# Optimization experiments

Hardware: AMD Instinct MI355X
Metric: run time of the kernel (lower is better)

Reference implementation:

```python
import jax, jax.numpy as jnp
import numpy as np

NUM_HEADS = 16
N_QUBITS = 8  # both attention d_k and FFN qubit count
LN_EPS = 1e-5


def setup_inputs() -> dict:
    key = jax.random.key(0)
    ks = jax.random.split(key, 8)
    B, S, E, F = 8, 4096, 128, 2048
    return {
        "x": jax.random.normal(ks[0], (B, S, E), dtype=jnp.float32),
        "theta_attn": jax.random.normal(ks[1], (N_QUBITS,), dtype=jnp.float32),
        "phi_ffn": jax.random.normal(ks[2], (N_QUBITS,), dtype=jnp.float32),
        "w1": jax.random.normal(ks[3], (F, N_QUBITS), dtype=jnp.float32) * (1.0 / np.sqrt(N_QUBITS)),
        "b1": jax.random.normal(ks[4], (F,), dtype=jnp.float32) * 0.01,
        "w2": jax.random.normal(ks[5], (E, F), dtype=jnp.float32) * (1.0 / np.sqrt(F)),
        "b2": jax.random.normal(ks[6], (E,), dtype=jnp.float32) * 0.01,
        "gamma1": jnp.ones((E,), dtype=jnp.float32),
        "beta1": jnp.zeros((E,), dtype=jnp.float32),
        "gamma2": jnp.ones((E,), dtype=jnp.float32),
        "beta2": jnp.zeros((E,), dtype=jnp.float32),
    }


def _layernorm(y, g, b):
    m = jnp.mean(y, axis=-1, keepdims=True)
    v = jnp.var(y, axis=-1, keepdims=True)
    return (y - m) * jax.lax.rsqrt(v + LN_EPS) * g + b


def _quantum_attn(x, theta):
    # RX(x_k)RX(theta_k) per wire -> per-wire <Z>=cos(x_k+theta_k); CNOT chain + ring
    # maps Z_j -> Z_0..Z_j (j>=1) and Z_0 -> Z_0..Z_{n-1} (Heisenberg picture),
    # so outputs are cumulative products of cosines within each head.
    B, S, E = x.shape
    a = x.reshape(B, S, NUM_HEADS, N_QUBITS) + theta  # (B,S,H,8)
    cp = jnp.cumprod(jnp.cos(a), axis=-1)
    out = jnp.concatenate([cp[..., -1:], cp[..., 1:]], axis=-1)  # wire0 gets full product
    return out.reshape(B, S, E)


def _quantum_ffn(x, phi):
    # RY(phi_j)RX(x_j)|0> -> <Z_j> = cos(phi_j)*cos(x_j); encoder only reads first N_QUBITS feats
    return jnp.cos(phi) * jnp.cos(x[..., :N_QUBITS])  # (B,S,8)


def reference(x, theta_attn, phi_ffn, w1, b1, w2, b2, gamma1, beta1, gamma2, beta2):
    attn = _quantum_attn(x, theta_attn)
    x1 = _layernorm(x + attn, gamma1, beta1)  # dropout is identity in eval
    q = _quantum_ffn(x1, phi_ffn)
    h = jax.nn.relu(jnp.einsum('bsq,fq->bsf', q, w1) + b1)
    ffn = jnp.einsum('bsf,ef->bse', h, w2) + b2
    return _layernorm(x1 + ffn, gamma2, beta2)
```

## Files before the change

### kernel.cpp

```cpp
#include <hip/hip_runtime.h>
#include <hip/hip_bf16.h>

typedef __attribute__((ext_vector_type(8))) short short8;
typedef __attribute__((ext_vector_type(4))) float f32x4;
typedef __attribute__((ext_vector_type(4))) int int4v;

#define LN_EPS 1e-5f

__device__ __forceinline__ unsigned short bf16rn(float f) {
    unsigned int u = __builtin_bit_cast(unsigned int, f);
    u = u + 0x7fffu + ((u >> 16) & 1u);
    return (unsigned short)(u >> 16);
}

__device__ __forceinline__ unsigned cvt_pk(float lo, float hi) {
    unsigned r;
    asm("v_cvt_pk_bf16_f32 %0, %1, %2" : "=v"(r) : "v"(lo), "v"(hi));
    return r;
}

__global__ __launch_bounds__(256) void k_prep(const float* __restrict__ w2,
                                              const float* __restrict__ w1,
                                              const float* __restrict__ b1,
                                              unsigned short* __restrict__ w2b,
                                              unsigned short* __restrict__ w1p) {
    const int bid = blockIdx.x;
    if (bid < 256) {
        int i = (bid * 256 + threadIdx.x) * 4;
        float4 v = *(const float4*)(w2 + i);
        ushort4 r;
        r.x = bf16rn(v.x); r.y = bf16rn(v.y); r.z = bf16rn(v.z); r.w = bf16rn(v.w);
        *(ushort4*)(w2b + i) = r;
    } else {
        int f = (bid - 256) * 256 + threadIdx.x;
        float4 wa = *(const float4*)(w1 + (size_t)f * 8);
        float4 wb = *(const float4*)(w1 + (size_t)f * 8 + 4);
        short8 r0, r1;
        r0[0] = (short)bf16rn(wa.x); r0[1] = (short)bf16rn(wa.y);
        r0[2] = (short)bf16rn(wa.z); r0[3] = (short)bf16rn(wa.w);
        r0[4] = (short)bf16rn(wb.x); r0[5] = (short)bf16rn(wb.y);
        r0[6] = (short)bf16rn(wb.z); r0[7] = (short)bf16rn(wb.w);
        r1 = short8{0, 0, 0, 0, 0, 0, 0, 0};
        r1[0] = (short)bf16rn(b1[f]);
        short8 z = short8{0, 0, 0, 0, 0, 0, 0, 0};
        unsigned short* row = w1p + (size_t)f * 32;
        *(short8*)(row) = r0;
        *(short8*)(row + 8) = r1;
        *(short8*)(row + 16) = z;
        *(short8*)(row + 24) = z;
    }
}

__global__ __launch_bounds__(256) void k_pre(const float* __restrict__ x,
                                             const float* __restrict__ theta,
                                             const float* __restrict__ phi,
                                             const float* __restrict__ gamma1,
                                             const float* __restrict__ beta1,
                                             float* __restrict__ x1,
                                             unsigned short* __restrict__ qpad) {
    const int tid = threadIdx.x;
    const int g = tid >> 4, li = tid & 15;
    const int tok = blockIdx.x * 16 + g;

    const float* xr = x + (size_t)tok * 128 + li * 8;
    float4 va = *(const float4*)xr;
    float4 vb = *(const float4*)(xr + 4);
    float v[8] = {va.x, va.y, va.z, va.w, vb.x, vb.y, vb.z, vb.w};

    float c[8];
#pragma unroll
    for (int k = 0; k < 8; ++k) c[k] = __cosf(v[k] + theta[k]);
    float cp[8];
    cp[0] = c[0];
#pragma unroll
    for (int k = 1; k < 8; ++k) cp[k] = cp[k - 1] * c[k];

    float y[8];
    y[0] = v[0] + cp[7];
#pragma unroll
    for (int k = 1; k < 8; ++k) y[k] = v[k] + cp[k];

    float s1 = 0.f, s2 = 0.f;
#pragma unroll
    for (int k = 0; k < 8; ++k) { s1 += y[k]; s2 += y[k] * y[k]; }
#pragma unroll
    for (int m = 1; m < 16; m <<= 1) {
        s1 += __shfl_xor(s1, m);
        s2 += __shfl_xor(s2, m);
    }
    float mean = s1 * (1.f / 128.f);
    float var = s2 * (1.f / 128.f) - mean * mean;
    float rs = rsqrtf(var + LN_EPS);

    float4 ga = *(const float4*)(gamma1 + li * 8);
    float4 gb = *(const float4*)(gamma1 + li * 8 + 4);
    float4 ba = *(const float4*)(beta1 + li * 8);
    float4 bb = *(const float4*)(beta1 + li * 8 + 4);
    float gam[8] = {ga.x, ga.y, ga.z, ga.w, gb.x, gb.y, gb.z, gb.w};
    float bet[8] = {ba.x, ba.y, ba.z, ba.w, bb.x, bb.y, bb.z, bb.w};

    float o[8];
#pragma unroll
    for (int k = 0; k < 8; ++k) o[k] = (y[k] - mean) * rs * gam[k] + bet[k];

    float* x1r = x1 + (size_t)tok * 128 + li * 8;
    *(float4*)x1r = make_float4(o[0], o[1], o[2], o[3]);
    *(float4*)(x1r + 4) = make_float4(o[4], o[5], o[6], o[7]);

    if (li == 0) {
        short8 qr;
#pragma unroll
        for (int k = 0; k < 8; ++k)
            qr[k] = (short)bf16rn(__cosf(phi[k]) * __cosf(o[k]));
        *(short8*)(qpad + (size_t)tok * 32) = qr;
    } else if (li < 4) {
        short8 z = short8{0, 0, 0, 0, 0, 0, 0, 0};
        if (li == 1) z[0] = (short)0x3F80;
        *(short8*)(qpad + (size_t)tok * 32 + li * 8) = z;
    }
}

__global__ __launch_bounds__(512, 4) void k_ffn(const float* __restrict__ x1,
                                                const unsigned short* __restrict__ qpad,
                                                const unsigned short* __restrict__ w2b,
                                                const unsigned short* __restrict__ w1p,
                                                const float* __restrict__ b2,
                                                const float* __restrict__ g2,
                                                const float* __restrict__ be2,
                                                float* __restrict__ out) {
    const int tid = threadIdx.x;
    const int wv = tid >> 6;
    const int kh = wv >> 2;
    const int sub = wv & 3;
    const int nh = sub & 1;
    const int mw = sub >> 1;
    const int lane = tid & 63;
    const int li = lane & 15;
    const int lg = lane >> 4;
    const int Tb = blockIdx.x * 64;
    const int lt0 = mw * 32;
    const int t0 = Tb + lt0;

    __shared__ __align__(16) char smem[65536 + 1024];
    unsigned short* Bs = (unsigned short*)smem;
    float (*red)[132] = (float(*)[132])smem;
    float (*sums)[4] = (float(*)[4])(smem + 65536);

    short8 qf[2];
#pragma unroll
    for (int mt = 0; mt < 2; ++mt)
        qf[mt] = *(const short8*)(qpad + (size_t)(t0 + mt * 16 + li) * 32 + lg * 8);

    const int arow0 = (8 * (li >> 2) + (li & 3)) * 32 + lg * 8;

    f32x4 acc[2][4];
#pragma unroll
    for (int mt = 0; mt < 2; ++mt)
#pragma unroll
        for (int nt = 0; nt < 4; ++nt) acc[mt][nt] = f32x4{0.f, 0.f, 0.f, 0.f};

    const int srow = lane >> 3;
    const int scs = (lane & 7) ^ srow;

    auto stage = [&](int buf, int kb_local) {
        const int kb = kh * 1024 + kb_local;
#pragma unroll
        for (int r = 0; r < 4; ++r) {
            const int e0 = r * 32 + sub * 8;
            const unsigned short* src =
                w2b + (size_t)(e0 + srow) * 2048 + kb + scs * 8;
            unsigned short* dst = Bs + (kh * 2 + buf) * 8192 + e0 * 64;
            __builtin_amdgcn_global_load_lds(
                (const __attribute__((address_space(1))) unsigned int*)src,
                (__attribute__((address_space(3))) unsigned int*)dst,
                16, 0, 0);
        }
    };

    stage(0, 0);
    __syncthreads();

    const f32x4 zero4 = f32x4{0.f, 0.f, 0.f, 0.f};

    for (int kbi = 0; kbi < 16; ++kbi) {
        const int buf = kbi & 1;
        if (kbi < 15) stage(buf ^ 1, (kbi + 1) * 64);

#pragma unroll
        for (int kk = 0; kk < 2; ++kk) {
            const int f = kh * 1024 + kbi * 64 + kk * 32;

            const unsigned short* wbase = w1p + (size_t)f * 32;
            short8 A0 = *(const short8*)(wbase + arow0);
            short8 A1 = *(const short8*)(wbase + arow0 + 128);

            const int cs = (kk * 4 + lg) ^ (li & 7);
            const unsigned short* basep =
                Bs + (kh * 2 + buf) * 8192 + (nh * 64 + li) * 64 + cs * 8;
            short8 bfr[4];
#pragma unroll
            for (int nt = 0; nt < 4; ++nt)
                bfr[nt] = *(const short8*)(basep + nt * 1024);

#pragma unroll
            for (int mt = 0; mt < 2; ++mt) {
                f32x4 p0 = __builtin_amdgcn_mfma_f32_16x16x32_bf16(A0, qf[mt], zero4, 0, 0, 0);
                f32x4 p1 = __builtin_amdgcn_mfma_f32_16x16x32_bf16(A1, qf[mt], zero4, 0, 0, 0);
#pragma unroll
                for (int r = 0; r < 4; ++r) {
                    p0[r] = fmaxf(p0[r], 0.f);
                    p1[r] = fmaxf(p1[r], 0.f);
                }
                int4v ai = {(int)cvt_pk(p0[0], p0[1]), (int)cvt_pk(p0[2], p0[3]),
                            (int)cvt_pk(p1[0], p1[1]), (int)cvt_pk(p1[2], p1[3])};
                short8 a2 = __builtin_bit_cast(short8, ai);
#pragma unroll
                for (int nt = 0; nt < 4; ++nt)
                    acc[mt][nt] = __builtin_amdgcn_mfma_f32_16x16x32_bf16(a2, bfr[nt], acc[mt][nt], 0, 0, 0);
            }
        }
        __syncthreads();
    }

    if (kh == 1) {
#pragma unroll
        for (int mt = 0; mt < 2; ++mt)
#pragma unroll
            for (int nt = 0; nt < 4; ++nt)
#pragma unroll
                for (int r = 0; r < 4; ++r)
                    red[lt0 + mt * 16 + lg * 4 + r][nh * 64 + nt * 16 + li] = acc[mt][nt][r];
    }
    __syncthreads();

    float b2v[4], g2v[4], be2v[4];
    if (kh == 0) {
#pragma unroll
        for (int nt = 0; nt < 4; ++nt) {
            int e = nh * 64 + nt * 16 + li;
            b2v[nt] = b2[e]; g2v[nt] = g2[e]; be2v[nt] = be2[e];
        }
#pragma unroll
        for (int mt = 0; mt < 2; ++mt) {
#pragma unroll
            for (int r = 0; r < 4; ++r) {
                const int ltok = lt0 + mt * 16 + lg * 4 + r;
                const int tok = Tb + ltok;
                const float* x1r = x1 + (size_t)tok * 128 + nh * 64 + li;
                float s1 = 0.f, s2 = 0.f;
#pragma unroll
                for (int nt = 0; nt < 4; ++nt) {
                    float v = acc[mt][nt][r] + red[ltok][nh * 64 + nt * 16 + li] +
                              b2v[nt] + x1r[nt * 16];
                    acc[mt][nt][r] = v;
                    s1 += v; s2 += v * v;
                }
#pragma unroll
                for (int m = 1; m < 16; m <<= 1) {
                    s1 += __shfl_xor(s1, m);
                    s2 += __shfl_xor(s2, m);
                }
                if (li == 0) {
                    sums[ltok][nh * 2 + 0] = s1;
                    sums[ltok][nh * 2 + 1] = s2;
                }
            }
        }
    }
    __syncthreads();

    if (kh == 0) {
#pragma unroll
        for (int mt = 0; mt < 2; ++mt) {
#pragma unroll
            for (int r = 0; r < 4; ++r) {
                const int ltok = lt0 + mt * 16 + lg * 4 + r;
                const int tok = Tb + ltok;
                float s1 = sums[ltok][0] + sums[ltok][2];
                float s2 = sums[ltok][1] + sums[ltok][3];
                float mean = s1 * (1.f / 128.f);
                float var = s2 * (1.f / 128.f) - mean * mean;
                float rs = rsqrtf(var + LN_EPS);
                float* orow = out + (size_t)tok * 128 + nh * 64 + li;
#pragma unroll
                for (int nt = 0; nt < 4; ++nt)
                    orow[nt * 16] = (acc[mt][nt][r] - mean) * rs * g2v[nt] + be2v[nt];
            }
        }
    }
}

extern "C" void kernel_launch(void* const* d_in, const int* in_sizes, int n_in,
                              void* d_out, int out_size, void* d_ws, size_t ws_size,
                              hipStream_t stream) {
    const float* x      = (const float*)d_in[0];
    const float* theta  = (const float*)d_in[1];
    const float* phi    = (const float*)d_in[2];
    const float* w1     = (const float*)d_in[3];
    const float* b1     = (const float*)d_in[4];
    const float* w2     = (const float*)d_in[5];
    const float* b2     = (const float*)d_in[6];
    const float* gamma1 = (const float*)d_in[7];
    const float* beta1  = (const float*)d_in[8];
    const float* gamma2 = (const float*)d_in[9];
    const float* beta2  = (const float*)d_in[10];
    float* out = (float*)d_out;

    char* ws = (char*)d_ws;
    unsigned short* w2b  = (unsigned short*)ws;
    unsigned short* w1p  = (unsigned short*)(ws + (512 << 10));
    unsigned short* qpad = (unsigned short*)(ws + (1 << 20));

    k_prep<<<264, 256, 0, stream>>>(w2, w1, b1, w2b, w1p);
    k_pre<<<2048, 256, 0, stream>>>(x, theta, phi, gamma1, beta1, out, qpad);
    k_ffn<<<512, 512, 0, stream>>>(out, qpad, w2b, w1p, b2, gamma2, beta2, out);
}
```

Measured before the change: 58.16 us.

## Merge weight prep into pre kernel and software-pipeline FFN A-fragment loads

```diff
diff --git a/kernel.cpp b/kernel.cpp
--- a/kernel.cpp
+++ b/kernel.cpp
@@ -17,38 +17,6 @@
     unsigned r;
     asm("v_cvt_pk_bf16_f32 %0, %1, %2" : "=v"(r) : "v"(lo), "v"(hi));
     return r;
-}
-
-__global__ __launch_bounds__(256) void k_prep(const float* __restrict__ w2,
-                                              const float* __restrict__ w1,
-                                              const float* __restrict__ b1,
-                                              unsigned short* __restrict__ w2b,
-                                              unsigned short* __restrict__ w1p) {
-    const int bid = blockIdx.x;
-    if (bid < 256) {
-        int i = (bid * 256 + threadIdx.x) * 4;
-        float4 v = *(const float4*)(w2 + i);
-        ushort4 r;
-        r.x = bf16rn(v.x); r.y = bf16rn(v.y); r.z = bf16rn(v.z); r.w = bf16rn(v.w);
-        *(ushort4*)(w2b + i) = r;
-    } else {
-        int f = (bid - 256) * 256 + threadIdx.x;
-        float4 wa = *(const float4*)(w1 + (size_t)f * 8);
-        float4 wb = *(const float4*)(w1 + (size_t)f * 8 + 4);
-        short8 r0, r1;
-        r0[0] = (short)bf16rn(wa.x); r0[1] = (short)bf16rn(wa.y);
-        r0[2] = (short)bf16rn(wa.z); r0[3] = (short)bf16rn(wa.w);
-        r0[4] = (short)bf16rn(wb.x); r0[5] = (short)bf16rn(wb.y);
-        r0[6] = (short)bf16rn(wb.z); r0[7] = (short)bf16rn(wb.w);
-        r1 = short8{0, 0, 0, 0, 0, 0, 0, 0};
-        r1[0] = (short)bf16rn(b1[f]);
-        short8 z = short8{0, 0, 0, 0, 0, 0, 0, 0};
-        unsigned short* row = w1p + (size_t)f * 32;
-        *(short8*)(row) = r0;
-        *(short8*)(row + 8) = r1;
-        *(short8*)(row + 16) = z;
-        *(short8*)(row + 24) = z;
-    }
 }
 
 __global__ __launch_bounds__(256) void k_pre(const float* __restrict__ x,
@@ -56,11 +24,47 @@
                                              const float* __restrict__ phi,
                                              const float* __restrict__ gamma1,
                                              const float* __restrict__ beta1,
+                                             const float* __restrict__ w1,
+                                             const float* __restrict__ b1,
+                                             const float* __restrict__ w2,
                                              float* __restrict__ x1,
-                                             unsigned short* __restrict__ qpad) {
+                                             unsigned short* __restrict__ qpad,
+                                             unsigned short* __restrict__ w2b,
+                                             unsigned short* __restrict__ w1p) {
     const int tid = threadIdx.x;
+    const int bid = blockIdx.x;
+
+    if (bid >= 2048) {
+        const int pid = bid - 2048;
+        if (pid < 256) {
+            int i = (pid * 256 + tid) * 4;
+            float4 v = *(const float4*)(w2 + i);
+            ushort4 r;
+            r.x = bf16rn(v.x); r.y = bf16rn(v.y); r.z = bf16rn(v.z); r.w = bf16rn(v.w);
+            *(ushort4*)(w2b + i) = r;
+        } else {
+            int f = (pid - 256) * 256 + tid;
+            float4 wa = *(const float4*)(w1 + (size_t)f * 8);
+            float4 wb = *(const float4*)(w1 + (size_t)f * 8 + 4);
+            short8 r0, r1;
+            r0[0] = (short)bf16rn(wa.x); r0[1] = (short)bf16rn(wa.y);
+            r0[2] = (short)bf16rn(wa.z); r0[3] = (short)bf16rn(wa.w);
+            r0[4] = (short)bf16rn(wb.x); r0[5] = (short)bf16rn(wb.y);
+            r0[6] = (short)bf16rn(wb.z); r0[7] = (short)bf16rn(wb.w);
+            r1 = short8{0, 0, 0, 0, 0, 0, 0, 0};
+            r1[0] = (short)bf16rn(b1[f]);
+            short8 z = short8{0, 0, 0, 0, 0, 0, 0, 0};
+            unsigned short* row = w1p + (size_t)f * 32;
+            *(short8*)(row) = r0;
+            *(short8*)(row + 8) = r1;
+            *(short8*)(row + 16) = z;
+            *(short8*)(row + 24) = z;
+        }
+        return;
+    }
+
     const int g = tid >> 4, li = tid & 15;
-    const int tok = blockIdx.x * 16 + g;
+    const int tok = bid * 16 + g;
 
     const float* xr = x + (size_t)tok * 128 + li * 8;
     float4 va = *(const float4*)xr;
@@ -177,26 +181,44 @@
         }
     };
 
+    short8 Areg[2][4];
+    auto loadA = [&](int kbi_, short8* dst) {
+#pragma unroll
+        for (int kk = 0; kk < 2; ++kk)
+#pragma unroll
+            for (int m = 0; m < 2; ++m)
+                dst[kk * 2 + m] = *(const short8*)(
+                    w1p + (size_t)(kh * 1024 + kbi_ * 64 + kk * 32) * 32 + arow0 + m * 128);
+    };
+
+    loadA(0, Areg[0]);
     stage(0, 0);
-    __syncthreads();
 
     const f32x4 zero4 = f32x4{0.f, 0.f, 0.f, 0.f};
 
+#pragma unroll
     for (int kbi = 0; kbi < 16; ++kbi) {
-        const int buf = kbi & 1;
-        if (kbi < 15) stage(buf ^ 1, (kbi + 1) * 64);
+        const int pcur = kbi & 1;
+        const int pnext = pcur ^ 1;
+
+        if (kbi < 15) {
+            loadA(kbi + 1, Areg[pnext]);
+            asm volatile("s_waitcnt vmcnt(4)" ::: "memory");
+        } else {
+            asm volatile("s_waitcnt vmcnt(0)" ::: "memory");
+        }
+        __builtin_amdgcn_s_barrier();
+        __builtin_amdgcn_sched_barrier(0);
+        if (kbi < 15) stage(pnext, (kbi + 1) * 64);
 
 #pragma unroll
         for (int kk = 0; kk < 2; ++kk) {
-            const int f = kh * 1024 + kbi * 64 + kk * 32;
-
-            const unsigned short* wbase = w1p + (size_t)f * 32;
-            short8 A0 = *(const short8*)(wbase + arow0);
-            short8 A1 = *(const short8*)(wbase + arow0 + 128);
+            short8 A0 = Areg[pcur][kk * 2 + 0];
+            short8 A1 = Areg[pcur][kk * 2 + 1];
 
             const int cs = (kk * 4 + lg) ^ (li & 7);
             const unsigned short* basep =
-                Bs + (kh * 2 + buf) * 8192 + (nh * 64 + li) * 64 + cs * 8;
+                Bs + (kh * 2 + pcur) * 8192 + (nh * 64 + li) * 64 + cs * 8;
             short8 bfr[4];
 #pragma unroll
             for (int nt = 0; nt < 4; ++nt)
@@ -219,8 +241,8 @@
                     acc[mt][nt] = __builtin_amdgcn_mfma_f32_16x16x32_bf16(a2, bfr[nt], acc[mt][nt], 0, 0, 0);
             }
         }
-        __syncthreads();
-    }
+    }
+    __syncthreads();
 
     if (kh == 1) {
 #pragma unroll
@@ -311,7 +333,7 @@
     unsigned short* w1p  = (unsigned short*)(ws + (512 << 10));
     unsigned short* qpad = (unsigned short*)(ws + (1 << 20));
 
-    k_prep<<<264, 256, 0, stream>>>(w2, w1, b1, w2b, w1p);
-    k_pre<<<2048, 256, 0, stream>>>(x, theta, phi, gamma1, beta1, out, qpad);
+    k_pre<<<2312, 256, 0, stream>>>(x, theta, phi, gamma1, beta1, w1, b1, w2,
+                                    out, qpad, w2b, w1p);
     k_ffn<<<512, 512, 0, stream>>>(out, qpad, w2b, w1p, b2, gamma2, beta2, out);
 }
```

Measured after the change: 51.04 us. 12.2% less time.
